# Kernel tuning notes

Measured on AMD Instinct MI355X. Metric: run time of the kernel, lower is better.

The kernel has to match this reference:

```python
import jax, jax.numpy as jnp
import numpy as np

N = 50000      # nodes
E = 800000     # edges
INS = 128
H = 128
OUTS = 128
G = 512        # graphs in batch
BN_EPS = 1e-5


def _lin(k, fan_in, fan_out):
    s = 1.0 / np.sqrt(fan_in)
    kw, kb = jax.random.split(k)
    w = jax.random.uniform(kw, (fan_in, fan_out), minval=-s, maxval=s, dtype=jnp.float32)
    b = jax.random.uniform(kb, (fan_out,), minval=-s, maxval=s, dtype=jnp.float32)
    return w, b


def setup_inputs() -> dict:
    key = jax.random.key(0)
    ks = jax.random.split(key, 16)
    x = jax.random.normal(ks[0], (N, INS), dtype=jnp.float32)
    edge_src = jax.random.randint(ks[1], (E,), 0, N, dtype=jnp.int32)
    edge_dst = jax.random.randint(ks[2], (E,), 0, N, dtype=jnp.int32)
    ptr = jnp.sort(jax.random.randint(ks[3], (G + 1,), 0, N, dtype=jnp.int32))
    ptr = ptr.at[0].set(0).at[-1].set(N)
    w1a, b1a = _lin(ks[4], INS, H)
    w1b, b1b = _lin(ks[5], H, H)
    w2a, b2a = _lin(ks[6], H, H)
    w2b, b2b = _lin(ks[7], H, H)
    w3a, b3a = _lin(ks[8], H, H)
    w3b, b3b = _lin(ks[9], H, OUTS)
    g1 = jnp.ones((H,), jnp.float32); be1 = jnp.zeros((H,), jnp.float32)
    g2 = jnp.ones((H,), jnp.float32); be2 = jnp.zeros((H,), jnp.float32)
    g3 = jnp.ones((H,), jnp.float32); be3 = jnp.zeros((H,), jnp.float32)
    return dict(x=x, edge_src=edge_src, edge_dst=edge_dst, ptr=ptr,
                w1a=w1a, b1a=b1a, g1=g1, be1=be1, w1b=w1b, b1b=b1b,
                w2a=w2a, b2a=b2a, g2=g2, be2=be2, w2b=w2b, b2b=b2b,
                w3a=w3a, b3a=b3a, g3=g3, be3=be3, w3b=w3b, b3b=b3b)


def _bn(h, gamma, beta):
    # BatchNorm1d in training mode: stats over the node dimension
    mu = jnp.mean(h, axis=0)
    var = jnp.var(h, axis=0)
    return gamma * (h - mu) * jax.lax.rsqrt(var + BN_EPS) + beta


def _gin_layer(h, src, dst, wa, ba, gamma, beta, wb, bb):
    # GINConv (eps=0): mlp(x + sum_{j in N(i)} x_j)
    agg = jax.ops.segment_sum(h[src], dst, num_segments=N)  # [N, d]
    h = h + agg
    h = jax.nn.relu(_bn(h @ wa + ba, gamma, beta))
    h = jax.nn.relu(h @ wb + bb)
    return h


def reference(x, edge_src, edge_dst, ptr,
              w1a, b1a, g1, be1, w1b, b1b,
              w2a, b2a, g2, be2, w2b, b2b,
              w3a, b3a, g3, be3, w3b, b3b):
    h = _gin_layer(x, edge_src, edge_dst, w1a, b1a, g1, be1, w1b, b1b)
    h = _gin_layer(h, edge_src, edge_dst, w2a, b2a, g2, be2, w2b, b2b)
    h = _gin_layer(h, edge_src, edge_dst, w3a, b3a, g3, be3, w3b, b3b)
    # segment_csr(x, ptr, reduce='sum') readout
    seg = jnp.searchsorted(ptr, jnp.arange(N, dtype=jnp.int32), side='right') - 1
    return jax.ops.segment_sum(h, seg, num_segments=G)  # [G, OUTS]
```

## Files before the change

### kernel.cpp

```cpp
#include <hip/hip_runtime.h>

#define NNODES 50000
#define NEDGES 800000
#define HD 128
#define NG 512
#define BN_EPS 1e-5f
#define GEMM_NB 391

typedef short bf16x8 __attribute__((ext_vector_type(8)));
typedef float floatx4 __attribute__((ext_vector_type(4)));

union U16 { uint4 u; bf16x8 h; };

__device__ __forceinline__ ushort f2bf(float f) {
    unsigned u = __float_as_uint(f);
    return (ushort)((u + 0x7fffu + ((u >> 16) & 1u)) >> 16);
}
__device__ __forceinline__ void unpack8(const uint4& u, float* f) {
    const unsigned* w = (const unsigned*)&u;
#pragma unroll
    for (int i = 0; i < 4; ++i) {
        f[2 * i]     = __uint_as_float(w[i] << 16);
        f[2 * i + 1] = __uint_as_float(w[i] & 0xffff0000u);
    }
}
__device__ __forceinline__ uint4 pack8(const float* f) {
    uint4 o;
    unsigned* w = (unsigned*)&o;
#pragma unroll
    for (int i = 0; i < 4; ++i)
        w[i] = (unsigned)f2bf(f[2 * i]) | ((unsigned)f2bf(f[2 * i + 1]) << 16);
    return o;
}


__global__ void hist_kernel(const int* __restrict__ dst, int* __restrict__ cnt, int n) {
    int i = blockIdx.x * 256 + threadIdx.x;
    if (i < n) atomicAdd(&cnt[dst[i]], 1);
}

__global__ void scan1_kernel(const int* __restrict__ cnt, int* __restrict__ incl,
                             int* __restrict__ bsum, int n) {
    __shared__ int s[1024];
    int i = blockIdx.x * 1024 + threadIdx.x;
    int v = (i < n) ? cnt[i] : 0;
    s[threadIdx.x] = v;
    __syncthreads();
    for (int off = 1; off < 1024; off <<= 1) {
        int add = (threadIdx.x >= off) ? s[threadIdx.x - off] : 0;
        __syncthreads();
        s[threadIdx.x] += add;
        __syncthreads();
    }
    if (i < n) incl[i] = s[threadIdx.x];
    if (threadIdx.x == 1023) bsum[blockIdx.x] = s[1023];
}

__global__ void scan2_kernel(const int* __restrict__ bsum, int* __restrict__ boffs, int nb) {
    __shared__ int s[64];
    int v = (threadIdx.x < nb) ? bsum[threadIdx.x] : 0;
    s[threadIdx.x] = v;
    __syncthreads();
    for (int off = 1; off < 64; off <<= 1) {
        int add = (threadIdx.x >= off) ? s[threadIdx.x - off] : 0;
        __syncthreads();
        s[threadIdx.x] += add;
        __syncthreads();
    }
    if (threadIdx.x < nb) boffs[threadIdx.x] = s[threadIdx.x] - v;
}

__global__ void scan3_kernel(const int* __restrict__ incl, const int* __restrict__ boffs,
                             int* __restrict__ rowp, int n) {
    int i = blockIdx.x * 256 + threadIdx.x;
    if (i < n) rowp[i + 1] = incl[i] + boffs[i >> 10];
    if (i == 0) rowp[0] = 0;
}

__global__ void build_kernel(const int* __restrict__ src, const int* __restrict__ dst,
                             const int* __restrict__ rowp, int* __restrict__ fill,
                             int* __restrict__ colv, int n) {
    int i = blockIdx.x * 256 + threadIdx.x;
    if (i < n) {
        int d = dst[i];
        int pos = rowp[d] + atomicAdd(&fill[d], 1);
        colv[pos] = src[i];
    }
}


__global__ void cvt_kernel(const float* __restrict__ x, ushort* __restrict__ xb, int n4) {
    int i = blockIdx.x * 256 + threadIdx.x;
    if (i < n4) {
        float4 v = ((const float4*)x)[i];
        ushort4 o;
        o.x = f2bf(v.x); o.y = f2bf(v.y); o.z = f2bf(v.z); o.w = f2bf(v.w);
        ((ushort4*)xb)[i] = o;
    }
}


struct WP6 { const float* w[6]; };

__global__ void wfrag_kernel(WP6 p, ushort* __restrict__ wf) {
    const float* W = p.w[blockIdx.x];
    ushort* o = wf + (size_t)blockIdx.x * 16384;
    for (int i = threadIdx.x; i < 16384; i += 256) {
        int j = i & 7, lane = (i >> 3) & 63, kc = (i >> 9) & 3, ct = i >> 11;
        int k = kc * 32 + (lane >> 4) * 8 + j;
        int n = ct * 16 + (lane & 15);
        o[i] = f2bf(W[k * HD + n]);
    }
}


__global__ __launch_bounds__(256) void aggregate_kernel(
    const ushort* __restrict__ h, const int* __restrict__ rowp,
    const int* __restrict__ colv, ushort* __restrict__ outv, int n) {
    int node = blockIdx.x * 16 + (threadIdx.x >> 4);
    int l = threadIdx.x & 15;
    if (node >= n) return;
    int beg = rowp[node], end = rowp[node + 1];
    const uint4* hp = (const uint4*)h;
    float a[8];
    uint4 sv = hp[(size_t)node * 16 + l];
    unpack8(sv, a);
    for (int j = beg; j < end; ++j) {
        uint4 v = hp[(size_t)colv[j] * 16 + l];
        float b[8];
        unpack8(v, b);
#pragma unroll
        for (int i = 0; i < 8; ++i) a[i] += b[i];
    }
    ((uint4*)outv)[(size_t)node * 16 + l] = pack8(a);
}


template <bool STATS, bool PRE_BN, bool READOUT>
__global__ __launch_bounds__(256, 3) void mfma_gemm_kernel(
    const ushort* __restrict__ A, const ushort* __restrict__ Wf,
    const float* __restrict__ bias, ushort* __restrict__ out,
    const float* __restrict__ gamma, const float* __restrict__ beta,
    float* __restrict__ ssum_p, float* __restrict__ ssq_p,
    const int* __restrict__ gptr, float* __restrict__ gout, int nrows) {
    __shared__ ushort bs[16384];
    __shared__ ushort cbuf[8192];
    __shared__ float reds[4][HD];
    __shared__ float redq[4][HD];
    __shared__ float sca[HD];
    __shared__ float shf[HD];
    const int t = threadIdx.x;
    const int wave = t >> 6, lane = t & 63;
    const int quad = lane >> 4, l16 = lane & 15;

    {
        const uint4* g = (const uint4*)Wf;
        uint4 v[8];
#pragma unroll
        for (int i = 0; i < 8; ++i) v[i] = g[i * 256 + t];
        uint4* s = (uint4*)bs;
#pragma unroll
        for (int i = 0; i < 8; ++i) s[i * 256 + t] = v[i];
    }

    if (PRE_BN && t < HD) {
        float s = 0.f, q = 0.f;
#pragma unroll
        for (int i = 0; i < 8; ++i) { s += ssum_p[i * HD + t]; q += ssq_p[i * HD + t]; }
        float mean = s / (float)nrows;
        float var = q / (float)nrows - mean * mean;
        float rstd = rsqrtf(var + BN_EPS);
        float sc = gamma[t] * rstd;
        sca[t] = sc;
        shf[t] = beta[t] - mean * sc;
    }

    uint4 a_cur[4];
    {
        int rowA = blockIdx.x * 64 + wave * 16 + l16;
        bool ok = rowA < nrows;
        const ushort* ap = A + (size_t)rowA * HD + quad * 8;
#pragma unroll
        for (int kc = 0; kc < 4; ++kc)
            a_cur[kc] = ok ? *(const uint4*)(ap + kc * 32) : make_uint4(0, 0, 0, 0);
    }

    __syncthreads();

    float s_acc[8], q_acc[8];
#pragma unroll
    for (int i = 0; i < 8; ++i) { s_acc[i] = 0.f; q_acc[i] = 0.f; }

    const uint4* B4 = (const uint4*)bs;
    floatx4 zf = {0.f, 0.f, 0.f, 0.f};

#pragma unroll
    for (int j = 0; j < 2; ++j) {
        const int tile = blockIdx.x + j * GEMM_NB;
        const int row0 = tile * 64;

        uint4 a_use[4];
#pragma unroll
        for (int kc = 0; kc < 4; ++kc) a_use[kc] = a_cur[kc];

        if (j == 0) {
            int rowA = (blockIdx.x + GEMM_NB) * 64 + wave * 16 + l16;
            bool ok = rowA < nrows;
            const ushort* ap = A + (size_t)rowA * HD + quad * 8;
#pragma unroll
            for (int kc = 0; kc < 4; ++kc)
                a_cur[kc] = ok ? *(const uint4*)(ap + kc * 32) : make_uint4(0, 0, 0, 0);
        }

        if (row0 < nrows) {
            floatx4 acc[8];
#pragma unroll
            for (int i = 0; i < 8; ++i) acc[i] = zf;

#pragma unroll
            for (int kc = 0; kc < 4; ++kc) {
                U16 au;
                au.u = a_use[kc];
                if (PRE_BN) {
                    float f[8];
                    unpack8(au.u, f);
                    int kb = kc * 32 + quad * 8;
                    float4 s0 = ((const float4*)(sca + kb))[0];
                    float4 s1 = ((const float4*)(sca + kb))[1];
                    float4 h0 = ((const float4*)(shf + kb))[0];
                    float4 h1 = ((const float4*)(shf + kb))[1];
                    f[0] = fmaxf(fmaf(f[0], s0.x, h0.x), 0.f);
                    f[1] = fmaxf(fmaf(f[1], s0.y, h0.y), 0.f);
                    f[2] = fmaxf(fmaf(f[2], s0.z, h0.z), 0.f);
                    f[3] = fmaxf(fmaf(f[3], s0.w, h0.w), 0.f);
                    f[4] = fmaxf(fmaf(f[4], s1.x, h1.x), 0.f);
                    f[5] = fmaxf(fmaf(f[5], s1.y, h1.y), 0.f);
                    f[6] = fmaxf(fmaf(f[6], s1.z, h1.z), 0.f);
                    f[7] = fmaxf(fmaf(f[7], s1.w, h1.w), 0.f);
                    au.u = pack8(f);
                }
#pragma unroll
                for (int ct = 0; ct < 8; ++ct) {
                    U16 bu;
                    bu.u = B4[(ct * 4 + kc) * 64 + lane];
                    acc[ct] = __builtin_amdgcn_mfma_f32_16x16x32_bf16(au.h, bu.h, acc[ct], 0, 0, 0);
                }
            }

            const int r_base = row0 + wave * 16 + quad * 4;

            if (READOUT) {
                int segr[4] = {-1, -1, -1, -1};
                if (r_base < nrows) {
                    int lo = 0, hi = NG - 1;
                    while (lo < hi) {
                        int mid = (lo + hi) >> 1;
                        if (r_base >= gptr[mid + 1]) lo = mid + 1; else hi = mid;
                    }
                    int sg = lo;
#pragma unroll
                    for (int reg = 0; reg < 4; ++reg) {
                        int rw = r_base + reg;
                        if (rw < nrows) {
                            while (rw >= gptr[sg + 1]) ++sg;
                            segr[reg] = sg;
                        }
                    }
                }
#pragma unroll
                for (int ct = 0; ct < 8; ++ct) {
                    int col = ct * 16 + l16;
                    float b = bias[col];
                    float run = 0.f;
                    int cur = segr[0];
#pragma unroll
                    for (int reg = 0; reg < 4; ++reg) {
                        if (segr[reg] != cur) {
                            if (cur >= 0 && run != 0.f) atomicAdd(&gout[cur * HD + col], run);
                            run = 0.f;
                            cur = segr[reg];
                        }
                        if (cur >= 0) run += fmaxf(acc[ct][reg] + b, 0.f);
                    }
                    if (cur >= 0 && run != 0.f) atomicAdd(&gout[cur * HD + col], run);
                }
            } else {
                const int lrow = wave * 16 + quad * 4;
#pragma unroll
                for (int ct = 0; ct < 8; ++ct) {
                    int col = ct * 16 + l16;
                    float b = bias[ct * 16 + l16];
#pragma unroll
                    for (int reg = 0; reg < 4; ++reg) {
                        float v = acc[ct][reg] + b;
                        if (!STATS) v = fmaxf(v, 0.f);
                        cbuf[(lrow + reg) * HD + col] = f2bf(v);
                        if (STATS && (r_base + reg) < nrows) {
                            s_acc[ct] += v;
                            q_acc[ct] += v * v;
                        }
                    }
                }
                __syncthreads();
                const uint4* c4 = (const uint4*)cbuf;
                uint4* o4 = (uint4*)out;
#pragma unroll
                for (int i = 0; i < 4; ++i) {
                    int f = t * 4 + i;
                    int row = f >> 4;
                    if (row0 + row < nrows) o4[(size_t)(row0 + row) * 16 + (f & 15)] = c4[f];
                }
                __syncthreads();
            }
        }
    }

    if (STATS) {
#pragma unroll
        for (int ct = 0; ct < 8; ++ct) {
            float s = s_acc[ct], q = q_acc[ct];
            s += __shfl_xor(s, 16); s += __shfl_xor(s, 32);
            q += __shfl_xor(q, 16); q += __shfl_xor(q, 32);
            if (quad == 0) { reds[wave][ct * 16 + l16] = s; redq[wave][ct * 16 + l16] = q; }
        }
        __syncthreads();
        int slot = (blockIdx.x & 7) * HD;
        if (t < HD) {
            atomicAdd(&ssum_p[slot + t], reds[0][t] + reds[1][t] + reds[2][t] + reds[3][t]);
        } else if (t < 2 * HD) {
            int c = t - HD;
            atomicAdd(&ssq_p[slot + c], redq[0][c] + redq[1][c] + redq[2][c] + redq[3][c]);
        }
    }
}


extern "C" void kernel_launch(void* const* d_in, const int* in_sizes, int n_in,
                              void* d_out, int out_size, void* d_ws, size_t ws_size,
                              hipStream_t stream) {
    const float* x = (const float*)d_in[0];
    const int* esrc = (const int*)d_in[1];
    const int* edst = (const int*)d_in[2];
    const int* gptr = (const int*)d_in[3];
    const float* wA[3] = {(const float*)d_in[4], (const float*)d_in[10], (const float*)d_in[16]};
    const float* bA[3] = {(const float*)d_in[5], (const float*)d_in[11], (const float*)d_in[17]};
    const float* gm[3] = {(const float*)d_in[6], (const float*)d_in[12], (const float*)d_in[18]};
    const float* bt[3] = {(const float*)d_in[7], (const float*)d_in[13], (const float*)d_in[19]};
    const float* wB[3] = {(const float*)d_in[8], (const float*)d_in[14], (const float*)d_in[20]};
    const float* bB[3] = {(const float*)d_in[9], (const float*)d_in[15], (const float*)d_in[21]};

    char* w = (char*)d_ws;
    ushort* xb   = (ushort*)w; w += (size_t)NNODES * HD * 2;
    ushort* tmpb = (ushort*)w; w += (size_t)NNODES * HD * 2;
    ushort* zbb  = (ushort*)w; w += (size_t)NNODES * HD * 2;
    ushort* hbb  = (ushort*)w; w += (size_t)NNODES * HD * 2;
    ushort* wf   = (ushort*)w; w += (size_t)6 * 16384 * 2;
    int* colv  = (int*)w;   w += (size_t)NEDGES * 4;
    int* incl  = (int*)w;   w += (size_t)NNODES * 4;
    int* rowp  = (int*)w;   w += ((size_t)(NNODES + 1) * 4 + 15) & ~(size_t)15;
    int* bsum  = (int*)w;   w += 64 * 4;
    int* boffs = (int*)w;   w += 64 * 4;
    char* zero_base = w;
    int* cnt   = (int*)w;   w += (size_t)NNODES * 4;
    int* fill  = (int*)w;   w += (size_t)NNODES * 4;
    float* ssum_p = (float*)w; w += 3 * 8 * 128 * 4;
    float* ssq_p  = (float*)w; w += 3 * 8 * 128 * 4;
    size_t zero_bytes = (size_t)(w - zero_base);

    hipMemsetAsync(zero_base, 0, zero_bytes, stream);
    hipMemsetAsync(d_out, 0, (size_t)NG * HD * 4, stream);

    hist_kernel<<<(NEDGES + 255) / 256, 256, 0, stream>>>(edst, cnt, NEDGES);
    int nsb = (NNODES + 1023) / 1024;
    scan1_kernel<<<nsb, 1024, 0, stream>>>(cnt, incl, bsum, NNODES);
    scan2_kernel<<<1, 64, 0, stream>>>(bsum, boffs, nsb);
    scan3_kernel<<<(NNODES + 255) / 256, 256, 0, stream>>>(incl, boffs, rowp, NNODES);
    build_kernel<<<(NEDGES + 255) / 256, 256, 0, stream>>>(esrc, edst, rowp, fill, colv, NEDGES);

    cvt_kernel<<<(NNODES * HD / 4 + 255) / 256, 256, 0, stream>>>(x, xb, NNODES * HD / 4);
    WP6 wp;
    wp.w[0] = wA[0]; wp.w[1] = wB[0]; wp.w[2] = wA[1];
    wp.w[3] = wB[1]; wp.w[4] = wA[2]; wp.w[5] = wB[2];
    wfrag_kernel<<<6, 256, 0, stream>>>(wp, wf);

    const int agg_grid = (NNODES + 15) / 16;
    const ushort* hin = xb;
    for (int l = 0; l < 3; ++l) {
        aggregate_kernel<<<agg_grid, 256, 0, stream>>>(hin, rowp, colv, tmpb, NNODES);
        mfma_gemm_kernel<true, false, false><<<GEMM_NB, 256, 0, stream>>>(
            tmpb, wf + (size_t)(2 * l) * 16384, bA[l], zbb, nullptr, nullptr,
            ssum_p + l * 1024, ssq_p + l * 1024, nullptr, nullptr, NNODES);
        if (l < 2) {
            mfma_gemm_kernel<false, true, false><<<GEMM_NB, 256, 0, stream>>>(
                zbb, wf + (size_t)(2 * l + 1) * 16384, bB[l], hbb, gm[l], bt[l],
                ssum_p + l * 1024, ssq_p + l * 1024, nullptr, nullptr, NNODES);
        } else {
            mfma_gemm_kernel<false, true, true><<<GEMM_NB, 256, 0, stream>>>(
                zbb, wf + (size_t)(2 * l + 1) * 16384, bB[l], nullptr, gm[l], bt[l],
                ssum_p + l * 1024, ssq_p + l * 1024, gptr, (float*)d_out, NNODES);
        }
        hin = hbb;
    }
}
```

Before: 434.1 us.

## Fuse neighbor aggregation into first GEMM and use one tile per block

```diff
diff --git a/kernel.cpp b/kernel.cpp
--- a/kernel.cpp
+++ b/kernel.cpp
@@ -5,7 +5,9 @@
 #define HD 128
 #define NG 512
 #define BN_EPS 1e-5f
-#define GEMM_NB 391
+#define GEMM_NB 782
+#define NSPLIT 16
+#define AROW 136
 
 typedef short bf16x8 __attribute__((ext_vector_type(8)));
 typedef float floatx4 __attribute__((ext_vector_type(4)));
@@ -114,44 +116,23 @@
 }
 
 
-__global__ __launch_bounds__(256) void aggregate_kernel(
-    const ushort* __restrict__ h, const int* __restrict__ rowp,
-    const int* __restrict__ colv, ushort* __restrict__ outv, int n) {
-    int node = blockIdx.x * 16 + (threadIdx.x >> 4);
-    int l = threadIdx.x & 15;
-    if (node >= n) return;
-    int beg = rowp[node], end = rowp[node + 1];
-    const uint4* hp = (const uint4*)h;
-    float a[8];
-    uint4 sv = hp[(size_t)node * 16 + l];
-    unpack8(sv, a);
-    for (int j = beg; j < end; ++j) {
-        uint4 v = hp[(size_t)colv[j] * 16 + l];
-        float b[8];
-        unpack8(v, b);
-#pragma unroll
-        for (int i = 0; i < 8; ++i) a[i] += b[i];
-    }
-    ((uint4*)outv)[(size_t)node * 16 + l] = pack8(a);
-}
-
-
-template <bool STATS, bool PRE_BN, bool READOUT>
-__global__ __launch_bounds__(256, 3) void mfma_gemm_kernel(
-    const ushort* __restrict__ A, const ushort* __restrict__ Wf,
-    const float* __restrict__ bias, ushort* __restrict__ out,
+template <bool GATHER, bool STATS, bool PRE_BN, bool READOUT>
+__global__ __launch_bounds__(256, 3) void fused_gemm_kernel(
+    const ushort* __restrict__ H, const int* __restrict__ rowp,
+    const int* __restrict__ colv,
+    const ushort* __restrict__ Wf, const float* __restrict__ bias,
+    ushort* __restrict__ out,
     const float* __restrict__ gamma, const float* __restrict__ beta,
     float* __restrict__ ssum_p, float* __restrict__ ssq_p,
     const int* __restrict__ gptr, float* __restrict__ gout, int nrows) {
     __shared__ ushort bs[16384];
-    __shared__ ushort cbuf[8192];
-    __shared__ float reds[4][HD];
-    __shared__ float redq[4][HD];
+    __shared__ ushort abuf[64 * AROW];
     __shared__ float sca[HD];
     __shared__ float shf[HD];
     const int t = threadIdx.x;
     const int wave = t >> 6, lane = t & 63;
     const int quad = lane >> 4, l16 = lane & 15;
+    const int row0 = blockIdx.x * 64;
 
     {
         const uint4* g = (const uint4*)Wf;
@@ -166,7 +147,7 @@
     if (PRE_BN && t < HD) {
         float s = 0.f, q = 0.f;
 #pragma unroll
-        for (int i = 0; i < 8; ++i) { s += ssum_p[i * HD + t]; q += ssq_p[i * HD + t]; }
+        for (int i = 0; i < NSPLIT; ++i) { s += ssum_p[i * HD + t]; q += ssq_p[i * HD + t]; }
         float mean = s / (float)nrows;
         float var = q / (float)nrows - mean * mean;
         float rstd = rsqrtf(var + BN_EPS);
@@ -176,10 +157,41 @@
     }
 
     uint4 a_cur[4];
-    {
-        int rowA = blockIdx.x * 64 + wave * 16 + l16;
+    if (GATHER) {
+        uint4* a4 = (uint4*)abuf;
+        const uint4* hp = (const uint4*)H;
+#pragma unroll
+        for (int half = 0; half < 2; ++half) {
+            int rl = half * 32 + (t >> 3);
+            int r = row0 + rl;
+            int p = t & 7;
+            float a[16];
+            if (r < nrows) {
+                size_t base = (size_t)r * 16 + p * 2;
+                uint4 v0 = hp[base], v1 = hp[base + 1];
+                unpack8(v0, a);
+                unpack8(v1, a + 8);
+                int beg = rowp[r], end = rowp[r + 1];
+                for (int j = beg; j < end; ++j) {
+                    size_t sb = (size_t)colv[j] * 16 + p * 2;
+                    uint4 w0 = hp[sb], w1 = hp[sb + 1];
+                    float b[16];
+                    unpack8(w0, b);
+                    unpack8(w1, b + 8);
+#pragma unroll
+                    for (int i = 0; i < 16; ++i) a[i] += b[i];
+                }
+            } else {
+#pragma unroll
+                for (int i = 0; i < 16; ++i) a[i] = 0.f;
+            }
+            a4[rl * (AROW / 8) + p * 2]     = pack8(a);
+            a4[rl * (AROW / 8) + p * 2 + 1] = pack8(a + 8);
+        }
+    } else {
+        int rowA = row0 + wave * 16 + l16;
         bool ok = rowA < nrows;
-        const ushort* ap = A + (size_t)rowA * HD + quad * 8;
+        const ushort* ap = H + (size_t)rowA * HD + quad * 8;
 #pragma unroll
         for (int kc = 0; kc < 4; ++kc)
             a_cur[kc] = ok ? *(const uint4*)(ap + kc * 32) : make_uint4(0, 0, 0, 0);
@@ -187,149 +199,140 @@
 
     __syncthreads();
 
-    float s_acc[8], q_acc[8];
-#pragma unroll
-    for (int i = 0; i < 8; ++i) { s_acc[i] = 0.f; q_acc[i] = 0.f; }
+    floatx4 zf = {0.f, 0.f, 0.f, 0.f};
+    floatx4 acc[8];
+#pragma unroll
+    for (int i = 0; i < 8; ++i) acc[i] = zf;
 
     const uint4* B4 = (const uint4*)bs;
-    floatx4 zf = {0.f, 0.f, 0.f, 0.f};
-
-#pragma unroll
-    for (int j = 0; j < 2; ++j) {
-        const int tile = blockIdx.x + j * GEMM_NB;
-        const int row0 = tile * 64;
-
-        uint4 a_use[4];
-#pragma unroll
-        for (int kc = 0; kc < 4; ++kc) a_use[kc] = a_cur[kc];
-
-        if (j == 0) {
-            int rowA = (blockIdx.x + GEMM_NB) * 64 + wave * 16 + l16;
-            bool ok = rowA < nrows;
-            const ushort* ap = A + (size_t)rowA * HD + quad * 8;
-#pragma unroll
-            for (int kc = 0; kc < 4; ++kc)
-                a_cur[kc] = ok ? *(const uint4*)(ap + kc * 32) : make_uint4(0, 0, 0, 0);
-        }
-
-        if (row0 < nrows) {
-            floatx4 acc[8];
-#pragma unroll
-            for (int i = 0; i < 8; ++i) acc[i] = zf;
-
-#pragma unroll
-            for (int kc = 0; kc < 4; ++kc) {
-                U16 au;
-                au.u = a_use[kc];
-                if (PRE_BN) {
-                    float f[8];
-                    unpack8(au.u, f);
-                    int kb = kc * 32 + quad * 8;
-                    float4 s0 = ((const float4*)(sca + kb))[0];
-                    float4 s1 = ((const float4*)(sca + kb))[1];
-                    float4 h0 = ((const float4*)(shf + kb))[0];
-                    float4 h1 = ((const float4*)(shf + kb))[1];
-                    f[0] = fmaxf(fmaf(f[0], s0.x, h0.x), 0.f);
-                    f[1] = fmaxf(fmaf(f[1], s0.y, h0.y), 0.f);
-                    f[2] = fmaxf(fmaf(f[2], s0.z, h0.z), 0.f);
-                    f[3] = fmaxf(fmaf(f[3], s0.w, h0.w), 0.f);
-                    f[4] = fmaxf(fmaf(f[4], s1.x, h1.x), 0.f);
-                    f[5] = fmaxf(fmaf(f[5], s1.y, h1.y), 0.f);
-                    f[6] = fmaxf(fmaf(f[6], s1.z, h1.z), 0.f);
-                    f[7] = fmaxf(fmaf(f[7], s1.w, h1.w), 0.f);
-                    au.u = pack8(f);
-                }
-#pragma unroll
-                for (int ct = 0; ct < 8; ++ct) {
-                    U16 bu;
-                    bu.u = B4[(ct * 4 + kc) * 64 + lane];
-                    acc[ct] = __builtin_amdgcn_mfma_f32_16x16x32_bf16(au.h, bu.h, acc[ct], 0, 0, 0);
+    const uint4* a4 = (const uint4*)abuf;
+    const int rowL = wave * 16 + l16;
+
+#pragma unroll
+    for (int kc = 0; kc < 4; ++kc) {
+        U16 au;
+        if (GATHER) {
+            au.u = a4[rowL * (AROW / 8) + kc * 4 + quad];
+        } else {
+            au.u = a_cur[kc];
+            if (PRE_BN) {
+                float f[8];
+                unpack8(au.u, f);
+                int kb = kc * 32 + quad * 8;
+                float4 s0 = ((const float4*)(sca + kb))[0];
+                float4 s1 = ((const float4*)(sca + kb))[1];
+                float4 h0 = ((const float4*)(shf + kb))[0];
+                float4 h1 = ((const float4*)(shf + kb))[1];
+                f[0] = fmaxf(fmaf(f[0], s0.x, h0.x), 0.f);
+                f[1] = fmaxf(fmaf(f[1], s0.y, h0.y), 0.f);
+                f[2] = fmaxf(fmaf(f[2], s0.z, h0.z), 0.f);
+                f[3] = fmaxf(fmaf(f[3], s0.w, h0.w), 0.f);
+                f[4] = fmaxf(fmaf(f[4], s1.x, h1.x), 0.f);
+                f[5] = fmaxf(fmaf(f[5], s1.y, h1.y), 0.f);
+                f[6] = fmaxf(fmaf(f[6], s1.z, h1.z), 0.f);
+                f[7] = fmaxf(fmaf(f[7], s1.w, h1.w), 0.f);
+                au.u = pack8(f);
+            }
+        }
+#pragma unroll
+        for (int ct = 0; ct < 8; ++ct) {
+            U16 bu;
+            bu.u = B4[(ct * 4 + kc) * 64 + lane];
+            acc[ct] = __builtin_amdgcn_mfma_f32_16x16x32_bf16(au.h, bu.h, acc[ct], 0, 0, 0);
+        }
+    }
+
+    const int r_base = row0 + wave * 16 + quad * 4;
+
+    if (READOUT) {
+        int segr[4] = {-1, -1, -1, -1};
+        if (r_base < nrows) {
+            int lo = 0, hi = NG - 1;
+            while (lo < hi) {
+                int mid = (lo + hi) >> 1;
+                if (r_base >= gptr[mid + 1]) lo = mid + 1; else hi = mid;
+            }
+            int sg = lo;
+#pragma unroll
+            for (int reg = 0; reg < 4; ++reg) {
+                int rw = r_base + reg;
+                if (rw < nrows) {
+                    while (rw >= gptr[sg + 1]) ++sg;
+                    segr[reg] = sg;
                 }
             }
-
-            const int r_base = row0 + wave * 16 + quad * 4;
-
-            if (READOUT) {
-                int segr[4] = {-1, -1, -1, -1};
-                if (r_base < nrows) {
-                    int lo = 0, hi = NG - 1;
-                    while (lo < hi) {
-                        int mid = (lo + hi) >> 1;
-                        if (r_base >= gptr[mid + 1]) lo = mid + 1; else hi = mid;
-                    }
-                    int sg = lo;
-#pragma unroll
-                    for (int reg = 0; reg < 4; ++reg) {
-                        int rw = r_base + reg;
-                        if (rw < nrows) {
-                            while (rw >= gptr[sg + 1]) ++sg;
-                            segr[reg] = sg;
-                        }
-                    }
+        }
+#pragma unroll
+        for (int ct = 0; ct < 8; ++ct) {
+            int col = ct * 16 + l16;
+            float b = bias[col];
+            float run = 0.f;
+            int cur = segr[0];
+#pragma unroll
+            for (int reg = 0; reg < 4; ++reg) {
+                if (segr[reg] != cur) {
+                    if (cur >= 0 && run != 0.f) atomicAdd(&gout[cur * HD + col], run);
+                    run = 0.f;
+                    cur = segr[reg];
                 }
-#pragma unroll
-                for (int ct = 0; ct < 8; ++ct) {
-                    int col = ct * 16 + l16;
-                    float b = bias[col];
-                    float run = 0.f;
-                    int cur = segr[0];
-#pragma unroll
-                    for (int reg = 0; reg < 4; ++reg) {
-                        if (segr[reg] != cur) {
-                            if (cur >= 0 && run != 0.f) atomicAdd(&gout[cur * HD + col], run);
-                            run = 0.f;
-                            cur = segr[reg];
-                        }
-                        if (cur >= 0) run += fmaxf(acc[ct][reg] + b, 0.f);
-                    }
-                    if (cur >= 0 && run != 0.f) atomicAdd(&gout[cur * HD + col], run);
-                }
-            } else {
-                const int lrow = wave * 16 + quad * 4;
-#pragma unroll
-                for (int ct = 0; ct < 8; ++ct) {
-                    int col = ct * 16 + l16;
-                    float b = bias[ct * 16 + l16];
-#pragma unroll
-                    for (int reg = 0; reg < 4; ++reg) {
-                        float v = acc[ct][reg] + b;
-                        if (!STATS) v = fmaxf(v, 0.f);
-                        cbuf[(lrow + reg) * HD + col] = f2bf(v);
-                        if (STATS && (r_base + reg) < nrows) {
-                            s_acc[ct] += v;
-                            q_acc[ct] += v * v;
-                        }
-                    }
-                }
-                __syncthreads();
-                const uint4* c4 = (const uint4*)cbuf;
-                uint4* o4 = (uint4*)out;
-#pragma unroll
-                for (int i = 0; i < 4; ++i) {
-                    int f = t * 4 + i;
-                    int row = f >> 4;
-                    if (row0 + row < nrows) o4[(size_t)(row0 + row) * 16 + (f & 15)] = c4[f];
-                }
-                __syncthreads();
+                if (cur >= 0) run += fmaxf(acc[ct][reg] + b, 0.f);
             }
-        }
-    }
-
+            if (cur >= 0 && run != 0.f) atomicAdd(&gout[cur * HD + col], run);
+        }
+        return;
+    }
+
+    float s_acc[8], q_acc[8];
+    const int lrow = wave * 16 + quad * 4;
+#pragma unroll
+    for (int ct = 0; ct < 8; ++ct) {
+        int col = ct * 16 + l16;
+        float b = bias[col];
+        float s = 0.f, q = 0.f;
+#pragma unroll
+        for (int reg = 0; reg < 4; ++reg) {
+            float v = acc[ct][reg] + b;
+            if (!STATS) v = fmaxf(v, 0.f);
+            abuf[(lrow + reg) * AROW + col] = f2bf(v);
+            if (STATS && (r_base + reg) < nrows) { s += v; q += v * v; }
+        }
+        s_acc[ct] = s; q_acc[ct] = q;
+    }
+
+    __syncthreads();
+
+    float* reds = (float*)bs;
+    float* redq = ((float*)bs) + 512;
     if (STATS) {
 #pragma unroll
         for (int ct = 0; ct < 8; ++ct) {
             float s = s_acc[ct], q = q_acc[ct];
             s += __shfl_xor(s, 16); s += __shfl_xor(s, 32);
             q += __shfl_xor(q, 16); q += __shfl_xor(q, 32);
-            if (quad == 0) { reds[wave][ct * 16 + l16] = s; redq[wave][ct * 16 + l16] = q; }
-        }
+            if (quad == 0) { reds[wave * HD + ct * 16 + l16] = s; redq[wave * HD + ct * 16 + l16] = q; }
+        }
+    }
+
+    {
+        const uint4* c4 = (const uint4*)abuf;
+        uint4* o4 = (uint4*)out;
+#pragma unroll
+        for (int i = 0; i < 4; ++i) {
+            int f = t * 4 + i;
+            int row = f >> 4;
+            int part = f & 15;
+            if (row0 + row < nrows) o4[(size_t)(row0 + row) * 16 + part] = c4[row * (AROW / 8) + part];
+        }
+    }
+
+    if (STATS) {
         __syncthreads();
-        int slot = (blockIdx.x & 7) * HD;
+        int slot = (blockIdx.x & (NSPLIT - 1)) * HD;
         if (t < HD) {
-            atomicAdd(&ssum_p[slot + t], reds[0][t] + reds[1][t] + reds[2][t] + reds[3][t]);
+            atomicAdd(&ssum_p[slot + t], reds[t] + reds[HD + t] + reds[2 * HD + t] + reds[3 * HD + t]);
         } else if (t < 2 * HD) {
             int c = t - HD;
-            atomicAdd(&ssq_p[slot + c], redq[0][c] + redq[1][c] + redq[2][c] + redq[3][c]);
+            atomicAdd(&ssq_p[slot + c], redq[c] + redq[HD + c] + redq[2 * HD + c] + redq[3 * HD + c]);
         }
     }
 }
@@ -351,7 +354,6 @@
 
     char* w = (char*)d_ws;
     ushort* xb   = (ushort*)w; w += (size_t)NNODES * HD * 2;
-    ushort* tmpb = (ushort*)w; w += (size_t)NNODES * HD * 2;
     ushort* zbb  = (ushort*)w; w += (size_t)NNODES * HD * 2;
     ushort* hbb  = (ushort*)w; w += (size_t)NNODES * HD * 2;
     ushort* wf   = (ushort*)w; w += (size_t)6 * 16384 * 2;
@@ -363,8 +365,8 @@
     char* zero_base = w;
     int* cnt   = (int*)w;   w += (size_t)NNODES * 4;
     int* fill  = (int*)w;   w += (size_t)NNODES * 4;
-    float* ssum_p = (float*)w; w += 3 * 8 * 128 * 4;
-    float* ssq_p  = (float*)w; w += 3 * 8 * 128 * 4;
+    float* ssum_p = (float*)w; w += 3 * NSPLIT * 128 * 4;
+    float* ssq_p  = (float*)w; w += 3 * NSPLIT * 128 * 4;
     size_t zero_bytes = (size_t)(w - zero_base);
 
     hipMemsetAsync(zero_base, 0, zero_bytes, stream);
@@ -383,21 +385,22 @@
     wp.w[3] = wB[1]; wp.w[4] = wA[2]; wp.w[5] = wB[2];
     wfrag_kernel<<<6, 256, 0, stream>>>(wp, wf);
 
-    const int agg_grid = (NNODES + 15) / 16;
     const ushort* hin = xb;
     for (int l = 0; l < 3; ++l) {
-        aggregate_kernel<<<agg_grid, 256, 0, stream>>>(hin, rowp, colv, tmpb, NNODES);
-        mfma_gemm_kernel<true, false, false><<<GEMM_NB, 256, 0, stream>>>(
-            tmpb, wf + (size_t)(2 * l) * 16384, bA[l], zbb, nullptr, nullptr,
-            ssum_p + l * 1024, ssq_p + l * 1024, nullptr, nullptr, NNODES);
+        fused_gemm_kernel<true, true, false, false><<<GEMM_NB, 256, 0, stream>>>(
+            hin, rowp, colv, wf + (size_t)(2 * l) * 16384, bA[l], zbb,
+            nullptr, nullptr, ssum_p + l * NSPLIT * 128, ssq_p + l * NSPLIT * 128,
+            nullptr, nullptr, NNODES);
         if (l < 2) {
-            mfma_gemm_kernel<false, true, false><<<GEMM_NB, 256, 0, stream>>>(
-                zbb, wf + (size_t)(2 * l + 1) * 16384, bB[l], hbb, gm[l], bt[l],
-                ssum_p + l * 1024, ssq_p + l * 1024, nullptr, nullptr, NNODES);
+            fused_gemm_kernel<false, false, true, false><<<GEMM_NB, 256, 0, stream>>>(
+                zbb, nullptr, nullptr, wf + (size_t)(2 * l + 1) * 16384, bB[l], hbb,
+                gm[l], bt[l], ssum_p + l * NSPLIT * 128, ssq_p + l * NSPLIT * 128,
+                nullptr, nullptr, NNODES);
         } else {
-            mfma_gemm_kernel<false, true, true><<<GEMM_NB, 256, 0, stream>>>(
-                zbb, wf + (size_t)(2 * l + 1) * 16384, bB[l], nullptr, gm[l], bt[l],
-                ssum_p + l * 1024, ssq_p + l * 1024, gptr, (float*)d_out, NNODES);
+            fused_gemm_kernel<false, false, true, true><<<GEMM_NB, 256, 0, stream>>>(
+                zbb, nullptr, nullptr, wf + (size_t)(2 * l + 1) * 16384, bB[l], nullptr,
+                gm[l], bt[l], ssum_p + l * NSPLIT * 128, ssq_p + l * NSPLIT * 128,
+                gptr, (float*)d_out, NNODES);
         }
         hin = hbb;
     }
```

After: 499.2 us. +15.0%, slower.
